# Performance work log

Hardware: AMD Instinct MI355X
Metric: run time of the kernel (lower is better)

## Reference

```python
import jax, jax.numpy as jnp
import numpy as np
from jax.scipy.linalg import solve_triangular

CHUNK = 32  # chunk_size default of _delta_rule_chunkwise


def setup_inputs() -> dict:
    key = jax.random.key(0)
    kq, kk, kv, kb = jax.random.split(key, 4)
    b, h, L, dk, dv = 4, 4, 4096, 256, 256
    return {
        "q": jax.random.normal(kq, (b, h, L, dk), jnp.float32),
        "k": jax.random.normal(kk, (b, h, L, dk), jnp.float32),
        "v": jax.random.normal(kv, (b, h, L, dv), jnp.float32),
        "beta": jax.random.uniform(kb, (b, h, L), jnp.float32),  # sigmoid output in (0,1)
    }


def reference(q, k, v, beta):
    c = CHUNK
    b, h, L, dk = q.shape
    dv = v.shape[-1]
    assert L % c == 0  # static shape chosen divisible; original pads otherwise
    n = L // c

    l2 = lambda x: x / jnp.linalg.norm(x, axis=-1, keepdims=True)
    q = l2(q)
    k = l2(k)
    v = v * beta[..., None]
    k_beta = k * beta[..., None]

    # split into chunks: [b,h,n,c,d]
    rc = lambda x: x.reshape(b, h, n, c, -1)
    qc, kc, vc, kbc = rc(q), rc(k), rc(v), rc(k_beta)

    # Triangular inverse: original per-row loop computes inv s.t.
    # (inv + I) = (I + strict_tril(k_beta @ k^T))^{-1}; use a unit-lower triangular solve.
    A = jnp.tril(jnp.einsum('bhncd,bhned->bhnce', kbc, kc), -1)  # strict lower [b,h,n,c,c]
    eye = jnp.eye(c, dtype=q.dtype)
    inv = solve_triangular(eye + A, jnp.broadcast_to(eye, A.shape), lower=True)

    u = inv @ vc        # [b,h,n,c,dv]
    w = inv @ kbc       # [b,h,n,c,dk]

    mask_low = jnp.tril(jnp.ones((c, c), dtype=q.dtype))  # keep lower incl. diag
    to_scan = lambda x: jnp.moveaxis(x, 2, 0)  # [n,b,h,c,d]

    def step(S, inp):
        q_i, k_i, u_i, w_i = inp
        att = jnp.einsum('bhcd,bhed->bhce', q_i, k_i) * mask_low
        u_adj = u_i - jnp.einsum('bhcd,bhde->bhce', w_i, S)
        o = jnp.einsum('bhcd,bhde->bhce', q_i, S) + att @ u_adj
        S = S + jnp.einsum('bhcd,bhce->bhde', k_i, u_adj)
        return S, o

    S0 = jnp.zeros((b, h, dk, dv), q.dtype)
    S, out = jax.lax.scan(step, S0, (to_scan(qc), to_scan(kc), to_scan(u), to_scan(w)))
    out = jnp.moveaxis(out, 0, 2).reshape(b, h, L, dv)
    return out, S
```

## Files before the change

kernel.cpp:

```cpp
#include <hip/hip_runtime.h>
#include <hip/hip_fp16.h>


typedef _Float16 half8 __attribute__((ext_vector_type(8)));
typedef float f32x4 __attribute__((ext_vector_type(4)));
typedef unsigned int u32x2 __attribute__((ext_vector_type(2)));
typedef unsigned int u32x4 __attribute__((ext_vector_type(4)));

__device__ __forceinline__ unsigned short f2h(float f) {
    return __half_as_ushort(__float2half(f));
}
__device__ __forceinline__ float h2f(unsigned short u) {
    return __half2float(__ushort_as_half(u));
}
__device__ __forceinline__ unsigned int pk2(float a, float b) {
    return (unsigned int)f2h(a) | ((unsigned int)f2h(b) << 16);
}

#define MFMA16(a, b, c) __builtin_amdgcn_mfma_f32_16x16x32_f16((a), (b), (c), 0, 0, 0)

__global__ __launch_bounds__(256, 2) void p1_kernel(
    const float* __restrict__ qg, const float* __restrict__ kg,
    const float* __restrict__ vg, const float* __restrict__ bg,
    unsigned short* __restrict__ qn_w, unsigned short* __restrict__ w_w,
    unsigned short* __restrict__ kT_w, unsigned short* __restrict__ u_w,
    unsigned short* __restrict__ att_w)
{
    __shared__ unsigned short kn_l[32][264];
    __shared__ unsigned short kb_l[32][264];
    __shared__ unsigned short qn_l[32][264];
    __shared__ float          A_l[32][34];
    __shared__ unsigned short att_l[32][40];
    __shared__ unsigned short wst[256][40];
    __shared__ float          beta_l[32];

    const int tid = threadIdx.x;
    const int g   = blockIdx.x;
    const int bh  = g >> 7;
    const int ci  = g & 127;
    const size_t inBase = ((size_t)bh * 4096 + (size_t)ci * 32) * 256;

    if (tid < 32) beta_l[tid] = bg[(size_t)bh * 4096 + ci * 32 + tid];

    const int r = tid >> 3, p = tid & 7, d0 = p * 32;
    const float bval = bg[(size_t)bh * 4096 + ci * 32 + r];

    {
        float vals[32]; float ss = 0.f;
        const float4* src = (const float4*)(kg + inBase + (size_t)r * 256 + d0);
        #pragma unroll
        for (int i = 0; i < 8; i++) {
            float4 v4 = src[i];
            vals[4*i+0] = v4.x; vals[4*i+1] = v4.y; vals[4*i+2] = v4.z; vals[4*i+3] = v4.w;
            ss += v4.x*v4.x + v4.y*v4.y + v4.z*v4.z + v4.w*v4.w;
        }
        ss += __shfl_xor(ss, 1); ss += __shfl_xor(ss, 2); ss += __shfl_xor(ss, 4);
        const float rn = rsqrtf(ss);
        unsigned int* dstn = (unsigned int*)&kn_l[r][d0];
        unsigned int* dstb = (unsigned int*)&kb_l[r][d0];
        #pragma unroll
        for (int i = 0; i < 16; i++) {
            float a = vals[2*i] * rn, b = vals[2*i+1] * rn;
            dstn[i] = pk2(a, b);
            dstb[i] = pk2(a * bval, b * bval);
        }
    }
    {
        float vals[32]; float ss = 0.f;
        const float4* src = (const float4*)(qg + inBase + (size_t)r * 256 + d0);
        #pragma unroll
        for (int i = 0; i < 8; i++) {
            float4 v4 = src[i];
            vals[4*i+0] = v4.x; vals[4*i+1] = v4.y; vals[4*i+2] = v4.z; vals[4*i+3] = v4.w;
            ss += v4.x*v4.x + v4.y*v4.y + v4.z*v4.z + v4.w*v4.w;
        }
        ss += __shfl_xor(ss, 1); ss += __shfl_xor(ss, 2); ss += __shfl_xor(ss, 4);
        const float rn = rsqrtf(ss);
        unsigned int pq[16];
        #pragma unroll
        for (int i = 0; i < 16; i++) pq[i] = pk2(vals[2*i] * rn, vals[2*i+1] * rn);
        unsigned int* dstq = (unsigned int*)&qn_l[r][d0];
        #pragma unroll
        for (int i = 0; i < 16; i++) dstq[i] = pq[i];
        u32x4* og = (u32x4*)(qn_w + ((size_t)g * 32 + r) * 256 + d0);
        #pragma unroll
        for (int m = 0; m < 4; m++) {
            u32x4 val; val.x = pq[4*m]; val.y = pq[4*m+1]; val.z = pq[4*m+2]; val.w = pq[4*m+3];
            og[m] = val;
        }
    }
    __syncthreads();

    {
        const int wid = tid >> 6, lane = tid & 63;
        const int mt = wid >> 1, ntt = wid & 1;
        const int l15 = lane & 15, l4 = lane >> 4;
        f32x4 accA = {0.f, 0.f, 0.f, 0.f}, accT = {0.f, 0.f, 0.f, 0.f};
        #pragma unroll
        for (int kk = 0; kk < 8; kk++) {
            half8 bfr = *(const half8*)&kn_l[ntt*16 + l15][kk*32 + l4*8];
            half8 afr = *(const half8*)&kb_l[mt*16 + l15][kk*32 + l4*8];
            half8 qfr = *(const half8*)&qn_l[mt*16 + l15][kk*32 + l4*8];
            accA = MFMA16(afr, bfr, accA);
            accT = MFMA16(qfr, bfr, accT);
        }
        #pragma unroll
        for (int j = 0; j < 4; j++) {
            int row = mt*16 + l4*4 + j, col = ntt*16 + l15;
            A_l[row][col]   = (row > col)  ? accA[j] : 0.f;
            att_l[row][col] = (row >= col) ? f2h(accT[j]) : (unsigned short)0;
        }
    }
    {
        const int dk = tid;
        unsigned short arr[32];
        #pragma unroll
        for (int j = 0; j < 32; j++) arr[j] = kn_l[j][dk];
        u32x4* dst = (u32x4*)(kT_w + ((size_t)g * 256 + dk) * 32);
        #pragma unroll
        for (int m = 0; m < 4; m++) {
            u32x4 val;
            val.x = (unsigned)arr[8*m+0] | ((unsigned)arr[8*m+1] << 16);
            val.y = (unsigned)arr[8*m+2] | ((unsigned)arr[8*m+3] << 16);
            val.z = (unsigned)arr[8*m+4] | ((unsigned)arr[8*m+5] << 16);
            val.w = (unsigned)arr[8*m+6] | ((unsigned)arr[8*m+7] << 16);
            dst[m] = val;
        }
    }
    __syncthreads();

    {
        const int c = tid;
        float xu[32], xw[32];
        #pragma unroll
        for (int j = 0; j < 32; j++) {
            xu[j] = vg[inBase + (size_t)j * 256 + c] * beta_l[j];
            xw[j] = h2f(kb_l[j][c]);
        }
        #pragma unroll
        for (int i = 1; i < 32; i++) {
            float su = xu[i], sw = xw[i];
            const float2* Ar = (const float2*)(&A_l[i][0]);
            #pragma unroll
            for (int h = 0; h < (i + 1) / 2; h++) {
                float2 a = Ar[h];
                su -= a.x * xu[2*h] + a.y * xu[2*h+1];
                sw -= a.x * xw[2*h] + a.y * xw[2*h+1];
            }
            xu[i] = su; xw[i] = sw;
        }
        unsigned int up[16];
        #pragma unroll
        for (int j = 0; j < 16; j++) up[j] = pk2(xu[2*j], xu[2*j+1]);
        u32x4* du = (u32x4*)(u_w + ((size_t)g * 256 + c) * 32);
        #pragma unroll
        for (int m = 0; m < 4; m++) {
            u32x4 val; val.x = up[4*m]; val.y = up[4*m+1]; val.z = up[4*m+2]; val.w = up[4*m+3];
            du[m] = val;
        }
        unsigned int* wd = (unsigned int*)&wst[c][0];
        #pragma unroll
        for (int j = 0; j < 16; j++) wd[j] = pk2(xw[2*j], xw[2*j+1]);
    }
    __syncthreads();

    {
        const int rr = tid >> 3, pp = tid & 7, dd0 = pp * 32;
        unsigned short arr[32];
        #pragma unroll
        for (int i = 0; i < 32; i++) arr[i] = wst[dd0 + i][rr];
        u32x4* dst = (u32x4*)(w_w + ((size_t)g * 32 + rr) * 256 + dd0);
        #pragma unroll
        for (int m = 0; m < 4; m++) {
            u32x4 val;
            val.x = (unsigned)arr[8*m+0] | ((unsigned)arr[8*m+1] << 16);
            val.y = (unsigned)arr[8*m+2] | ((unsigned)arr[8*m+3] << 16);
            val.z = (unsigned)arr[8*m+4] | ((unsigned)arr[8*m+5] << 16);
            val.w = (unsigned)arr[8*m+6] | ((unsigned)arr[8*m+7] << 16);
            dst[m] = val;
        }
    }
    if (tid < 128) {
        const int rr = tid >> 2, j0 = (tid & 3) * 8;
        u32x4 vv = *(const u32x4*)&att_l[rr][j0];
        *(u32x4*)(att_w + (size_t)g * 1024 + rr * 32 + j0) = vv;
    }
}

__global__ __launch_bounds__(256, 1) void p2_kernel(
    const unsigned short* __restrict__ qn_w, const unsigned short* __restrict__ w_w,
    const unsigned short* __restrict__ kT_w, const unsigned short* __restrict__ u_w,
    const unsigned short* __restrict__ att_w, float* __restrict__ outp)
{
    __shared__ unsigned short S_cm[32][264];
    __shared__ unsigned short uadj[32][40];

    const int tid = threadIdx.x;
    const int bid = blockIdx.x;
    const int bh  = bid & 15;
    const int dvb = bid >> 4;
    const int dv0 = dvb * 32;
    const int wid = tid >> 6, lane = tid & 63;
    const int mh  = wid >> 1;
    const int ntw = wid & 1;
    const int l15 = lane & 15, l4 = lane >> 4;

    for (int i = tid; i < 32 * 264 / 2; i += 256) ((unsigned int*)S_cm)[i] = 0u;

    f32x4 accS[8];
    #pragma unroll
    for (int d = 0; d < 8; d++) accS[d] = (f32x4){0.f, 0.f, 0.f, 0.f};

    const unsigned short* wqbase = mh ? qn_w : w_w;

    half8 wqA[8], wqB[8];
    {
        const size_t g0 = (size_t)bh * 128;
        #pragma unroll
        for (int kk = 0; kk < 8; kk++) {
            wqA[kk] = *(const half8*)(wqbase + (g0*32 +      l15) * 256 + kk*32 + l4*8);
            wqB[kk] = *(const half8*)(wqbase + (g0*32 + 16 + l15) * 256 + kk*32 + l4*8);
        }
    }
    __syncthreads();

    for (int t = 0; t < 128; ++t) {
        const size_t g = (size_t)bh * 128 + t;

        half8 kfrag[8];
        #pragma unroll
        for (int dt = 0; dt < 8; dt++)
            kfrag[dt] = *(const half8*)(kT_w + (g*256 + mh*128 + dt*16 + l15) * 32 + l4*8);
        half8 att0 = {}, att1 = {};
        u32x2 u0 = {}, u1 = {};
        if (mh) {
            att0 = *(const half8*)(att_w + (g*32 +      l15) * 32 + l4*8);
            att1 = *(const half8*)(att_w + (g*32 + 16 + l15) * 32 + l4*8);
        } else {
            u0 = *(const u32x2*)(u_w + (g*256 + dv0 + ntw*16 + l15) * 32 +      l4*4);
            u1 = *(const u32x2*)(u_w + (g*256 + dv0 + ntw*16 + l15) * 32 + 16 + l4*4);
        }

        f32x4 acc0 = {0.f,0.f,0.f,0.f}, acc1 = {0.f,0.f,0.f,0.f};
        #pragma unroll
        for (int kk = 0; kk < 8; kk++) {
            half8 b = *(const half8*)&S_cm[ntw*16 + l15][kk*32 + l4*8];
            acc0 = MFMA16(wqA[kk], b, acc0);
            acc1 = MFMA16(wqB[kk], b, acc1);
        }
        if (!mh) {
            u32x2 w0, w1;
            w0.x = pk2(h2f((unsigned short)(u0.x & 0xffff)) - acc0[0],
                       h2f((unsigned short)(u0.x >> 16))    - acc0[1]);
            w0.y = pk2(h2f((unsigned short)(u0.y & 0xffff)) - acc0[2],
                       h2f((unsigned short)(u0.y >> 16))    - acc0[3]);
            w1.x = pk2(h2f((unsigned short)(u1.x & 0xffff)) - acc1[0],
                       h2f((unsigned short)(u1.x >> 16))    - acc1[1]);
            w1.y = pk2(h2f((unsigned short)(u1.y & 0xffff)) - acc1[2],
                       h2f((unsigned short)(u1.y >> 16))    - acc1[3]);
            *(u32x2*)&uadj[ntw*16 + l15][l4*4]      = w0;
            *(u32x2*)&uadj[ntw*16 + l15][16 + l4*4] = w1;
        }
        __syncthreads();

        if (t < 127) {
            const size_t g2 = g + 1;
            #pragma unroll
            for (int kk = 0; kk < 8; kk++) {
                wqA[kk] = *(const half8*)(wqbase + (g2*32 +      l15) * 256 + kk*32 + l4*8);
                wqB[kk] = *(const half8*)(wqbase + (g2*32 + 16 + l15) * 256 + kk*32 + l4*8);
            }
        }

        half8 ub = *(const half8*)&uadj[ntw*16 + l15][l4*8];
        #pragma unroll
        for (int dt = 0; dt < 8; dt++) accS[dt] = MFMA16(kfrag[dt], ub, accS[dt]);

        if (mh) {
            acc0 = MFMA16(att0, ub, acc0);
            acc1 = MFMA16(att1, ub, acc1);
            const size_t ob = ((size_t)bh * 4096 + (size_t)t * 32) * 256 + dv0 + ntw*16 + l15;
            #pragma unroll
            for (int j = 0; j < 4; j++) {
                outp[ob + (size_t)(l4*4 + j) * 256]      = acc0[j];
                outp[ob + (size_t)(16 + l4*4 + j) * 256] = acc1[j];
            }
        }
        #pragma unroll
        for (int dt = 0; dt < 8; dt++) {
            u32x2 sw;
            sw.x = pk2(accS[dt][0], accS[dt][1]);
            sw.y = pk2(accS[dt][2], accS[dt][3]);
            *(u32x2*)&S_cm[ntw*16 + l15][mh*128 + dt*16 + l4*4] = sw;
        }
        __syncthreads();
    }

    const size_t sb = (size_t)16777216 + ((size_t)bh * 256) * 256 + dv0 + ntw*16 + l15;
    #pragma unroll
    for (int dt = 0; dt < 8; dt++) {
        #pragma unroll
        for (int j = 0; j < 4; j++)
            outp[sb + (size_t)(mh*128 + dt*16 + l4*4 + j) * 256] = accS[dt][j];
    }
}

extern "C" void kernel_launch(void* const* d_in, const int* in_sizes, int n_in,
                              void* d_out, int out_size, void* d_ws, size_t ws_size,
                              hipStream_t stream)
{
    (void)in_sizes; (void)n_in; (void)out_size; (void)ws_size;
    const float* q    = (const float*)d_in[0];
    const float* k    = (const float*)d_in[1];
    const float* v    = (const float*)d_in[2];
    const float* beta = (const float*)d_in[3];
    float* out = (float*)d_out;

    unsigned short* ws  = (unsigned short*)d_ws;
    const size_t SZ = (size_t)2048 * 32 * 256;
    unsigned short* qn  = ws;
    unsigned short* ww  = ws + SZ;
    unsigned short* kT  = ws + 2 * SZ;
    unsigned short* uu  = ws + 3 * SZ;
    unsigned short* att = ws + 4 * SZ;

    p1_kernel<<<2048, 256, 0, stream>>>(q, k, v, beta, qn, ww, kT, uu, att);
    p2_kernel<<<128, 256, 0, stream>>>(qn, ww, kT, uu, att, out);
}
```

Measured before the change: 920.2 us.

## Run scan kernel as single-wave blocks over 16-column dv slices

The sequential scan kernel now launches 256 single-wavefront blocks, each owning a 16-wide dv slice, instead of 128 four-wave blocks with 32-wide slices. Because each block is a single wavefront, the two __syncthreads barriers per chunk step go away, and S and u_adj live in XOR-swizzled LDS written and read by that one wave. Each wave computes both the W·S and Q·S products and the full 256-row state update. This doubles parallelism across CUs and removes barrier cost, at the price of more registers per wave (16 state accumulators plus fragments) and loss of the register prefetch of the next chunk's W/Q fragments.

```diff
diff --git a/kernel.cpp b/kernel.cpp
--- a/kernel.cpp
+++ b/kernel.cpp
@@ -187,121 +187,121 @@
     }
 }
 
-__global__ __launch_bounds__(256, 1) void p2_kernel(
+__global__ __launch_bounds__(64, 1) void p2_kernel(
     const unsigned short* __restrict__ qn_w, const unsigned short* __restrict__ w_w,
     const unsigned short* __restrict__ kT_w, const unsigned short* __restrict__ u_w,
     const unsigned short* __restrict__ att_w, float* __restrict__ outp)
 {
-    __shared__ unsigned short S_cm[32][264];
-    __shared__ unsigned short uadj[32][40];
-
-    const int tid = threadIdx.x;
-    const int bid = blockIdx.x;
-    const int bh  = bid & 15;
-    const int dvb = bid >> 4;
-    const int dv0 = dvb * 32;
-    const int wid = tid >> 6, lane = tid & 63;
-    const int mh  = wid >> 1;
-    const int ntw = wid & 1;
-    const int l15 = lane & 15, l4 = lane >> 4;
-
-    for (int i = tid; i < 32 * 264 / 2; i += 256) ((unsigned int*)S_cm)[i] = 0u;
-
-    f32x4 accS[8];
+    __shared__ unsigned short Sb[16 * 256];
+    __shared__ unsigned short Ub[16 * 32];
+
+    const int bid  = blockIdx.x;
+    const int bh   = bid & 15;
+    const int dv0  = (bid >> 4) * 16;
+    const int lane = threadIdx.x & 63;
+    const int l15  = lane & 15, l4 = lane >> 4;
+    const int sswz = (l15 & 7) << 3;
+    const int uswz = (l15 & 3) << 3;
+
+    unsigned short* SbR = Sb + l15 * 256;
+    unsigned short* UbR = Ub + l15 * 32;
+
+    f32x4 accS[16];
     #pragma unroll
-    for (int d = 0; d < 8; d++) accS[d] = (f32x4){0.f, 0.f, 0.f, 0.f};
-
-    const unsigned short* wqbase = mh ? qn_w : w_w;
-
-    half8 wqA[8], wqB[8];
-    {
-        const size_t g0 = (size_t)bh * 128;
-        #pragma unroll
-        for (int kk = 0; kk < 8; kk++) {
-            wqA[kk] = *(const half8*)(wqbase + (g0*32 +      l15) * 256 + kk*32 + l4*8);
-            wqB[kk] = *(const half8*)(wqbase + (g0*32 + 16 + l15) * 256 + kk*32 + l4*8);
-        }
-    }
-    __syncthreads();
-
+    for (int dt = 0; dt < 16; dt++) {
+        accS[dt] = (f32x4){0.f, 0.f, 0.f, 0.f};
+        u32x2 z; z.x = 0u; z.y = 0u;
+        *(u32x2*)&SbR[(dt*16 + l4*4) ^ sswz] = z;
+    }
+
+    #pragma unroll 1
     for (int t = 0; t < 128; ++t) {
         const size_t g = (size_t)bh * 128 + t;
-
-        half8 kfrag[8];
-        #pragma unroll
-        for (int dt = 0; dt < 8; dt++)
-            kfrag[dt] = *(const half8*)(kT_w + (g*256 + mh*128 + dt*16 + l15) * 32 + l4*8);
-        half8 att0 = {}, att1 = {};
-        u32x2 u0 = {}, u1 = {};
-        if (mh) {
-            att0 = *(const half8*)(att_w + (g*32 +      l15) * 32 + l4*8);
-            att1 = *(const half8*)(att_w + (g*32 + 16 + l15) * 32 + l4*8);
-        } else {
-            u0 = *(const u32x2*)(u_w + (g*256 + dv0 + ntw*16 + l15) * 32 +      l4*4);
-            u1 = *(const u32x2*)(u_w + (g*256 + dv0 + ntw*16 + l15) * 32 + 16 + l4*4);
-        }
-
-        f32x4 acc0 = {0.f,0.f,0.f,0.f}, acc1 = {0.f,0.f,0.f,0.f};
-        #pragma unroll
-        for (int kk = 0; kk < 8; kk++) {
-            half8 b = *(const half8*)&S_cm[ntw*16 + l15][kk*32 + l4*8];
-            acc0 = MFMA16(wqA[kk], b, acc0);
-            acc1 = MFMA16(wqB[kk], b, acc1);
-        }
-        if (!mh) {
-            u32x2 w0, w1;
-            w0.x = pk2(h2f((unsigned short)(u0.x & 0xffff)) - acc0[0],
-                       h2f((unsigned short)(u0.x >> 16))    - acc0[1]);
-            w0.y = pk2(h2f((unsigned short)(u0.y & 0xffff)) - acc0[2],
-                       h2f((unsigned short)(u0.y >> 16))    - acc0[3]);
-            w1.x = pk2(h2f((unsigned short)(u1.x & 0xffff)) - acc1[0],
-                       h2f((unsigned short)(u1.x >> 16))    - acc1[1]);
-            w1.y = pk2(h2f((unsigned short)(u1.y & 0xffff)) - acc1[2],
-                       h2f((unsigned short)(u1.y >> 16))    - acc1[3]);
-            *(u32x2*)&uadj[ntw*16 + l15][l4*4]      = w0;
-            *(u32x2*)&uadj[ntw*16 + l15][16 + l4*4] = w1;
-        }
-        __syncthreads();
-
-        if (t < 127) {
-            const size_t g2 = g + 1;
-            #pragma unroll
-            for (int kk = 0; kk < 8; kk++) {
-                wqA[kk] = *(const half8*)(wqbase + (g2*32 +      l15) * 256 + kk*32 + l4*8);
-                wqB[kk] = *(const half8*)(wqbase + (g2*32 + 16 + l15) * 256 + kk*32 + l4*8);
-            }
-        }
-
-        half8 ub = *(const half8*)&uadj[ntw*16 + l15][l4*8];
-        #pragma unroll
-        for (int dt = 0; dt < 8; dt++) accS[dt] = MFMA16(kfrag[dt], ub, accS[dt]);
-
-        if (mh) {
-            acc0 = MFMA16(att0, ub, acc0);
-            acc1 = MFMA16(att1, ub, acc1);
-            const size_t ob = ((size_t)bh * 4096 + (size_t)t * 32) * 256 + dv0 + ntw*16 + l15;
-            #pragma unroll
-            for (int j = 0; j < 4; j++) {
-                outp[ob + (size_t)(l4*4 + j) * 256]      = acc0[j];
-                outp[ob + (size_t)(16 + l4*4 + j) * 256] = acc1[j];
-            }
-        }
-        #pragma unroll
-        for (int dt = 0; dt < 8; dt++) {
-            u32x2 sw;
-            sw.x = pk2(accS[dt][0], accS[dt][1]);
-            sw.y = pk2(accS[dt][2], accS[dt][3]);
-            *(u32x2*)&S_cm[ntw*16 + l15][mh*128 + dt*16 + l4*4] = sw;
-        }
-        __syncthreads();
-    }
-
-    const size_t sb = (size_t)16777216 + ((size_t)bh * 256) * 256 + dv0 + ntw*16 + l15;
+        const size_t rowQW = (g * 32 + l15) * 256 + l4 * 8;
+        const size_t rowK  = (g * 256 + l15) * 32 + l4 * 8;
+        const size_t rowU  = (g * 256 + dv0 + l15) * 32 + l4 * 4;
+
+        half8 sB[8];
+        #pragma unroll
+        for (int kk = 0; kk < 8; kk++)
+            sB[kk] = *(const half8*)&SbR[(kk*32 + l4*8) ^ sswz];
+
+        half8 wf0[8], wf1[8];
+        #pragma unroll
+        for (int kk = 0; kk < 8; kk++) {
+            wf0[kk] = *(const half8*)(w_w + rowQW + kk*32);
+            wf1[kk] = *(const half8*)(w_w + rowQW + 16*256 + kk*32);
+        }
+        u32x2 uc0 = *(const u32x2*)(u_w + rowU);
+        u32x2 uc1 = *(const u32x2*)(u_w + rowU + 16);
+        half8 kf[16];
+        #pragma unroll
+        for (int dt = 0; dt < 16; dt++)
+            kf[dt] = *(const half8*)(kT_w + rowK + (size_t)dt * 16 * 32);
+
+        f32x4 aW0 = {0.f,0.f,0.f,0.f}, aW1 = {0.f,0.f,0.f,0.f};
+        #pragma unroll
+        for (int kk = 0; kk < 8; kk++) {
+            aW0 = MFMA16(wf0[kk], sB[kk], aW0);
+            aW1 = MFMA16(wf1[kk], sB[kk], aW1);
+        }
+
+        u32x2 p0, p1;
+        p0.x = pk2(h2f((unsigned short)(uc0.x & 0xffff)) - aW0[0],
+                   h2f((unsigned short)(uc0.x >> 16))    - aW0[1]);
+        p0.y = pk2(h2f((unsigned short)(uc0.y & 0xffff)) - aW0[2],
+                   h2f((unsigned short)(uc0.y >> 16))    - aW0[3]);
+        p1.x = pk2(h2f((unsigned short)(uc1.x & 0xffff)) - aW1[0],
+                   h2f((unsigned short)(uc1.x >> 16))    - aW1[1]);
+        p1.y = pk2(h2f((unsigned short)(uc1.y & 0xffff)) - aW1[2],
+                   h2f((unsigned short)(uc1.y >> 16))    - aW1[3]);
+        *(u32x2*)&UbR[(l4*4) ^ uswz]      = p0;
+        *(u32x2*)&UbR[(16 + l4*4) ^ uswz] = p1;
+        half8 ub = *(const half8*)&UbR[(l4*8) ^ uswz];
+
+        half8 qf0[8], qf1[8];
+        #pragma unroll
+        for (int kk = 0; kk < 8; kk++) {
+            qf0[kk] = *(const half8*)(qn_w + rowQW + kk*32);
+            qf1[kk] = *(const half8*)(qn_w + rowQW + 16*256 + kk*32);
+        }
+        half8 af0 = *(const half8*)(att_w + g*1024 + (size_t)l15 * 32 + l4*8);
+        half8 af1 = *(const half8*)(att_w + g*1024 + (size_t)(16 + l15) * 32 + l4*8);
+
+        #pragma unroll
+        for (int dt = 0; dt < 16; dt++)
+            accS[dt] = MFMA16(kf[dt], ub, accS[dt]);
+
+        #pragma unroll
+        for (int dt = 0; dt < 16; dt++) {
+            u32x2 sp;
+            sp.x = pk2(accS[dt][0], accS[dt][1]);
+            sp.y = pk2(accS[dt][2], accS[dt][3]);
+            *(u32x2*)&SbR[(dt*16 + l4*4) ^ sswz] = sp;
+        }
+
+        f32x4 aQ0 = {0.f,0.f,0.f,0.f}, aQ1 = {0.f,0.f,0.f,0.f};
+        #pragma unroll
+        for (int kk = 0; kk < 8; kk++) {
+            aQ0 = MFMA16(qf0[kk], sB[kk], aQ0);
+            aQ1 = MFMA16(qf1[kk], sB[kk], aQ1);
+        }
+        aQ0 = MFMA16(af0, ub, aQ0);
+        aQ1 = MFMA16(af1, ub, aQ1);
+        float* ob = outp + ((size_t)bh * 4096 + (size_t)t * 32) * 256 + dv0 + l15;
+        #pragma unroll
+        for (int j = 0; j < 4; j++) {
+            ob[(size_t)(l4*4 + j) * 256]      = aQ0[j];
+            ob[(size_t)(16 + l4*4 + j) * 256] = aQ1[j];
+        }
+    }
+
+    float* so = outp + (size_t)16777216 + ((size_t)bh * 256) * 256 + dv0 + l15;
     #pragma unroll
-    for (int dt = 0; dt < 8; dt++) {
+    for (int dt = 0; dt < 16; dt++) {
         #pragma unroll
         for (int j = 0; j < 4; j++)
-            outp[sb + (size_t)(mh*128 + dt*16 + l4*4 + j) * 256] = accS[dt][j];
+            so[(size_t)(dt*16 + l4*4 + j) * 256] = accS[dt][j];
     }
 }
 
@@ -325,5 +325,5 @@
     unsigned short* att = ws + 4 * SZ;
 
     p1_kernel<<<2048, 256, 0, stream>>>(q, k, v, beta, qn, ww, kT, uu, att);
-    p2_kernel<<<128, 256, 0, stream>>>(qn, ww, kT, uu, att, out);
-}
+    p2_kernel<<<256, 64, 0, stream>>>(qn, ww, kT, uu, att, out);
+}
```

Result: slower. 1.428 ms (+55.2%).
